# Kernel tuning notes

Hardware: AMD Instinct MI355X
Metric: run time of the kernel (lower is better)

The kernel has to match this reference:

```python
import jax, jax.numpy as jnp
import numpy as np

N, E, IN_F, OUT_F, HEADS = 50000, 800000, 256, 64, 8


def setup_inputs() -> dict:
    key = jax.random.key(0)
    k1, k2, k3, k4, k5 = jax.random.split(key, 5)
    stdv = 1.0 / np.sqrt(OUT_F)
    return {
        "h": jax.random.normal(k1, (N, IN_F), dtype=jnp.float32),
        "weight": jax.random.uniform(k2, (IN_F, OUT_F), minval=-stdv, maxval=stdv, dtype=jnp.float32),
        "attention_w": jax.random.normal(k3, (1, HEADS), dtype=jnp.float32),
        "src": jax.random.randint(k4, (E,), 0, N, dtype=jnp.int32),
        "dst": jax.random.randint(k5, (E,), 0, N, dtype=jnp.int32),
    }


def reference(h, weight, attention_w, src, dst):
    n_nodes = h.shape[0]
    hp = h @ weight                              # [N, F] projected features
    hs = hp[src]                                 # [E, F] gather source feats
    hd = hp[dst]                                 # [E, F] gather dest feats
    dot = jnp.sum(hs * hd, axis=-1, keepdims=True)   # [E, 1] edge dot attention
    # original: (msg[:, F, 1] @ attention_w[1, H]).sum(H) == msg * attention_w.sum()
    msg = dot * hs * jnp.sum(attention_w)        # [E, F]
    accum = jax.ops.segment_sum(msg, dst, num_segments=n_nodes)  # [N, F]
    # DGL update_all: zero in-degree nodes keep their projected feature
    deg = jax.ops.segment_sum(jnp.ones((src.shape[0], 1), hp.dtype), dst, num_segments=n_nodes)
    return jnp.where(deg > 0, accum, hp)
```

## Files before the change

### kernel.cpp

```cpp
#include <hip/hip_runtime.h>

#define IN_F 256
#define OUT_F 64
#define NBKT_MAX 1024
#define PART_BLOCKS 128
#define HIST_BLOCKS 256
#define CAP 3072

typedef __attribute__((ext_vector_type(8))) short short8;
typedef __attribute__((ext_vector_type(4))) float f32x4;
typedef unsigned int uint32;

#define AS_I(f) __builtin_bit_cast(int, f)
#define AS_F(i) __builtin_bit_cast(float, i)
#define DPP_ADD(v, ctrl, rmask) \
    v += AS_F(__builtin_amdgcn_update_dpp(0, AS_I(v), ctrl, rmask, 0xf, true))

__device__ __forceinline__ float half_sum_sel(float p, bool hi) {
    DPP_ADD(p, 0x111, 0xf);
    DPP_ADD(p, 0x112, 0xf);
    DPP_ADD(p, 0x114, 0xf);
    DPP_ADD(p, 0x118, 0xf);
    DPP_ADD(p, 0x142, 0xa);
    float dlo = AS_F(__builtin_amdgcn_readlane(AS_I(p), 31));
    float dhi = AS_F(__builtin_amdgcn_readlane(AS_I(p), 63));
    return hi ? dhi : dlo;
}

__device__ __forceinline__ unsigned short f2bf(float f) {
    uint32 u = __builtin_bit_cast(uint32, f);
    u += 0x7fffu + ((u >> 16) & 1u);
    return (unsigned short)(u >> 16);
}
__device__ __forceinline__ float bf2f(unsigned short s) {
    return __builtin_bit_cast(float, (uint32)s << 16);
}

__global__ __launch_bounds__(256) void gemm_hist_kernel(const float* __restrict__ h,
                                                        const float* __restrict__ w,
                                                        unsigned short* __restrict__ hpb,
                                                        int N,
                                                        const int* __restrict__ dst,
                                                        int* __restrict__ bkt_cnt,
                                                        int E, int NB, int ngemm) {
    __shared__ char smem[32768];
    int b = blockIdx.x, t = threadIdx.x;

    if (b >= ngemm) {
        int* lcnt = (int*)smem;
        int hb = b - ngemm;
        for (int i = t; i < NB; i += 256) lcnt[i] = 0;
        __syncthreads();
        for (int e = hb * 256 + t; e < E; e += HIST_BLOCKS * 256)
            atomicAdd(&lcnt[dst[e] >> 6], 1);
        __syncthreads();
        for (int i = t; i < NB; i += 256)
            if (lcnt[i]) atomicAdd(&bkt_cnt[i], lcnt[i]);
        return;
    }

    short8* wfrag = (short8*)smem;
    for (int slot = t; slot < 2048; slot += 256) {
        int kb = slot >> 6, n = slot & 63;
        short8 v;
#pragma unroll
        for (int jj = 0; jj < 8; ++jj)
            v[jj] = (short)f2bf(w[(size_t)(kb * 8 + jj) * OUT_F + n]);
        wfrag[slot] = v;
    }
    __syncthreads();

    int wave = t >> 6, lane = t & 63;
    int n16  = lane & 15, quad = lane >> 4;
    int base = b * 64 + wave * 16;
    int arow_i = base + n16; if (arow_i >= N) arow_i = N - 1;
    const float* arow = h + (size_t)arow_i * IN_F;

    f32x4 acc[4];
#pragma unroll
    for (int ct = 0; ct < 4; ++ct) acc[ct] = (f32x4){0.f, 0.f, 0.f, 0.f};

#pragma unroll
    for (int ks = 0; ks < 8; ++ks) {
        int k0 = ks * 32;
        float4 a0 = *(const float4*)(arow + k0 + quad * 8);
        float4 a1 = *(const float4*)(arow + k0 + quad * 8 + 4);
        short8 af;
        af[0] = (short)f2bf(a0.x); af[1] = (short)f2bf(a0.y);
        af[2] = (short)f2bf(a0.z); af[3] = (short)f2bf(a0.w);
        af[4] = (short)f2bf(a1.x); af[5] = (short)f2bf(a1.y);
        af[6] = (short)f2bf(a1.z); af[7] = (short)f2bf(a1.w);
        int kb = ks * 4 + quad;
#pragma unroll
        for (int ct = 0; ct < 4; ++ct) {
            short8 bf = wfrag[kb * 64 + ct * 16 + n16];
            acc[ct] = __builtin_amdgcn_mfma_f32_16x16x32_bf16(af, bf, acc[ct], 0, 0, 0);
        }
    }

#pragma unroll
    for (int ct = 0; ct < 4; ++ct) {
#pragma unroll
        for (int r = 0; r < 4; ++r) {
            int ro = base + quad * 4 + r;
            if (ro < N) hpb[(size_t)ro * OUT_F + ct * 16 + n16] = f2bf(acc[ct][r]);
        }
    }
}

__global__ __launch_bounds__(512) void partition_kernel(const int* __restrict__ src,
                                                        const int* __restrict__ dst,
                                                        const int* __restrict__ bkt_cnt,
                                                        int* __restrict__ bkt_cursor,
                                                        int* __restrict__ bkt_base,
                                                        uint32* __restrict__ pairs,
                                                        int E, int NB) {
    __shared__ int sbase[NBKT_MAX + 1];
    __shared__ int lcnt[NBKT_MAX];
    __shared__ int gbase[NBKT_MAX];
    __shared__ int wsum2[8];

    int t = threadIdx.x, lane = t & 63, wid = t >> 6;

    int loc0, loc1;
    int x0 = (t * 2     < NB) ? bkt_cnt[t * 2]     : 0;
    int x1 = (t * 2 + 1 < NB) ? bkt_cnt[t * 2 + 1] : 0;
    loc0 = 0; loc1 = x0;
    int s = x0 + x1;
    int xs = s;
#pragma unroll
    for (int off = 1; off < 64; off <<= 1) {
        int y = __shfl_up(xs, off, 64);
        if (lane >= off) xs += y;
    }
    if (lane == 63) wsum2[wid] = xs;
    __syncthreads();
    int base_w = 0;
    for (int k = 0; k < wid; ++k) base_w += wsum2[k];
    int toff = base_w + xs - s;
    if (t * 2     < NB) sbase[t * 2]     = toff + loc0;
    if (t * 2 + 1 < NB) sbase[t * 2 + 1] = toff + loc1;
    if (t == 0) sbase[NB] = E;
    __syncthreads();

    if (blockIdx.x == 0) {
        for (int i = t; i <= NB; i += 512) bkt_base[i] = sbase[i];
    }

    int chunk = (E + PART_BLOCKS - 1) / PART_BLOCKS;
    int s0 = blockIdx.x * chunk;
    int s1 = min(E, s0 + chunk);

    for (int i = t; i < NB; i += 512) lcnt[i] = 0;
    __syncthreads();
    for (int e = s0 + t; e < s1; e += 512)
        atomicAdd(&lcnt[dst[e] >> 6], 1);
    __syncthreads();
    for (int i = t; i < NB; i += 512) {
        int c = lcnt[i];
        if (c) gbase[i] = sbase[i] + atomicAdd(&bkt_cursor[i], c);
        lcnt[i] = 0;
    }
    __syncthreads();
    for (int e = s0 + t; e < s1; e += 512) {
        int d  = dst[e];
        int bk = d >> 6;
        int idx = atomicAdd(&lcnt[bk], 1);
        pairs[gbase[bk] + idx] = (uint32)src[e] | ((uint32)(d & 63) << 26);
    }
}

#define GATH(S) (*(const uint32*)(hpb + (size_t)(S) * OUT_F + half * 2))
#define PROC(Q) { float a0 = bf2f((unsigned short)((Q) & 0xffff));            \
                  float a1 = bf2f((unsigned short)((Q) >> 16));               \
                  float dd = half_sum_sel(fmaf(a1, hd1, a0 * hd0), hi);       \
                  acc0 = fmaf(dd, a0, acc0); acc1 = fmaf(dd, a1, acc1); }

__global__ __launch_bounds__(512) void accum_sort_kernel(const unsigned short* __restrict__ hpb,
                                                         const uint32* __restrict__ pairs,
                                                         const int* __restrict__ bkt_base,
                                                         const float* __restrict__ attw,
                                                         float* __restrict__ out, int N) {
    __shared__ int slds[CAP];
    __shared__ int bin[64], excl[65], cur[64];

    int b = blockIdx.x, t = threadIdx.x;
    int wid = t >> 6, lane = t & 63;
    int half = lane & 31;
    bool hi  = lane >= 32;
    int node0 = b * 64;

    int beg = bkt_base[b], end = bkt_base[b + 1];
    int nE  = end - beg;

    float c = 0.f;
#pragma unroll
    for (int i = 0; i < 8; ++i) c += attw[i];

    if (nE <= CAP) {
        if (t < 64) bin[t] = 0;
        __syncthreads();
        for (int i = beg + t; i < end; i += 512)
            atomicAdd(&bin[pairs[i] >> 26], 1);
        __syncthreads();
        if (t < 64) {
            int v = bin[t], x = v;
#pragma unroll
            for (int off = 1; off < 64; off <<= 1) {
                int y = __shfl_up(x, off, 64);
                if (t >= off) x += y;
            }
            excl[t] = x - v;
            cur[t]  = x - v;
            if (t == 63) excl[64] = x;
        }
        __syncthreads();
        for (int i = beg + t; i < end; i += 512) {
            uint32 p = pairs[i];
            int dl   = (int)(p >> 26);
            int pos  = atomicAdd(&cur[dl], 1);
            slds[pos] = (int)(p & 0x3FFFFFFu);
        }
        __syncthreads();

#pragma unroll 1
        for (int k = 0; k < 8; ++k) {
            int n    = wid + 8 * k;
            int node = node0 + n;
            if (node >= N) continue;

            int jb = excl[n], je = excl[n + 1];

            uint32 hd2 = *(const uint32*)(hpb + (size_t)node * OUT_F + half * 2);
            float hd0 = bf2f((unsigned short)(hd2 & 0xffff));
            float hd1 = bf2f((unsigned short)(hd2 >> 16));

            float acc0 = 0.f, acc1 = 0.f;
            int j = jb;
            int sel = hi ? 1 : 0;

            for (; j + 16 <= je; j += 16) {
                int i0 = slds[j + 0  + sel], i1 = slds[j + 2  + sel];
                int i2 = slds[j + 4  + sel], i3 = slds[j + 6  + sel];
                int i4 = slds[j + 8  + sel], i5 = slds[j + 10 + sel];
                int i6 = slds[j + 12 + sel], i7 = slds[j + 14 + sel];
                uint32 q0 = GATH(i0), q1 = GATH(i1), q2 = GATH(i2), q3 = GATH(i3);
                uint32 q4 = GATH(i4), q5 = GATH(i5), q6 = GATH(i6), q7 = GATH(i7);
                PROC(q0) PROC(q1) PROC(q2) PROC(q3)
                PROC(q4) PROC(q5) PROC(q6) PROC(q7)
            }
            for (; j + 8 <= je; j += 8) {
                int i0 = slds[j + 0 + sel], i1 = slds[j + 2 + sel];
                int i2 = slds[j + 4 + sel], i3 = slds[j + 6 + sel];
                uint32 q0 = GATH(i0), q1 = GATH(i1), q2 = GATH(i2), q3 = GATH(i3);
                PROC(q0) PROC(q1) PROC(q2) PROC(q3)
            }
            for (; j + 2 <= je; j += 2) {
                int i0 = slds[j + sel];
                uint32 q0 = GATH(i0);
                PROC(q0)
            }
            if (j < je) {
                int i0 = slds[j];
                uint32 q0 = GATH(i0);
                float a0 = bf2f((unsigned short)(q0 & 0xffff));
                float a1 = bf2f((unsigned short)(q0 >> 16));
                float dd = half_sum_sel(fmaf(a1, hd1, a0 * hd0), false);
                if (!hi) {
                    acc0 = fmaf(dd, a0, acc0);
                    acc1 = fmaf(dd, a1, acc1);
                }
            }

            acc0 += __shfl_xor(acc0, 32, 64);
            acc1 += __shfl_xor(acc1, 32, 64);

            if (!hi) {
                float r0, r1;
                if (je > jb) { r0 = acc0 * c; r1 = acc1 * c; }
                else         { r0 = hd0;      r1 = hd1;      }
                *(float2*)(out + (size_t)node * OUT_F + half * 2) = make_float2(r0, r1);
            }
        }
    } else {
#pragma unroll 1
        for (int k = 0; k < 8; ++k) {
            int n    = wid + 8 * k;
            int node = node0 + n;
            if (node >= N) continue;

            uint32 hd2 = *(const uint32*)(hpb + (size_t)node * OUT_F + half * 2);
            float hd0 = bf2f((unsigned short)(hd2 & 0xffff));
            float hd1 = bf2f((unsigned short)(hd2 >> 16));

            float acc0 = 0.f, acc1 = 0.f;
            int deg = 0;
            for (int i = beg; i < end; ++i) {
                uint32 p = pairs[i];
                if ((int)(p >> 26) == n) {
                    ++deg;
                    uint32 q0 = GATH((int)(p & 0x3FFFFFFu));
                    float a0 = bf2f((unsigned short)(q0 & 0xffff));
                    float a1 = bf2f((unsigned short)(q0 >> 16));
                    float dd = half_sum_sel(fmaf(a1, hd1, a0 * hd0), false);
                    if (!hi) {
                        acc0 = fmaf(dd, a0, acc0);
                        acc1 = fmaf(dd, a1, acc1);
                    }
                }
            }
            acc0 += __shfl_xor(acc0, 32, 64);
            acc1 += __shfl_xor(acc1, 32, 64);
            if (!hi) {
                float r0, r1;
                if (deg > 0) { r0 = acc0 * c; r1 = acc1 * c; }
                else         { r0 = hd0;      r1 = hd1;      }
                *(float2*)(out + (size_t)node * OUT_F + half * 2) = make_float2(r0, r1);
            }
        }
    }
}

extern "C" void kernel_launch(void* const* d_in, const int* in_sizes, int n_in,
                              void* d_out, int out_size, void* d_ws, size_t ws_size,
                              hipStream_t stream) {
    const float* h    = (const float*)d_in[0];
    const float* w    = (const float*)d_in[1];
    const float* attw = (const float*)d_in[2];
    const int*   src  = (const int*)d_in[3];
    const int*   dst  = (const int*)d_in[4];

    int N = in_sizes[0] / IN_F;
    int E = in_sizes[3];
    int NB = (N + 63) >> 6;
    int ngemm = (N + 63) / 64;

    float* out = (float*)d_out;

    char* p = (char*)d_ws;
    unsigned short* hpb = (unsigned short*)p;  p += (size_t)N * OUT_F * sizeof(unsigned short);
    int* bkt_cnt    = (int*)p;                 p += (NBKT_MAX + 1) * sizeof(int);
    int* bkt_cursor = (int*)p;                 p += (NBKT_MAX + 1) * sizeof(int);
    int* bkt_base   = (int*)p;                 p += (NBKT_MAX + 1) * sizeof(int);
    uint32* pairs   = (uint32*)p;

    hipMemsetAsync(bkt_cnt, 0, 2 * (NBKT_MAX + 1) * sizeof(int), stream);

    gemm_hist_kernel<<<ngemm + HIST_BLOCKS, 256, 0, stream>>>(h, w, hpb, N,
                                                              dst, bkt_cnt, E, NB, ngemm);

    partition_kernel<<<PART_BLOCKS, 512, 0, stream>>>(src, dst, bkt_cnt, bkt_cursor,
                                                      bkt_base, pairs, E, NB);

    accum_sort_kernel<<<NB, 512, 0, stream>>>(hpb, pairs, bkt_base, attw, out, N);
}
```

Baseline: 154.8 us.

## Fuse partitioning into GEMM kernel with per-block local bucket tables

Replaces the global histogram, memset and separate partition kernel with a block-local partition inside the GEMM launch. Each of the 128 partition blocks sorts its own edge chunk by bucket and writes a per-block offset table. The accumulation kernel then gathers its bucket's 128 segments into LDS using a prefix sum and binary search. This removes a memset and one kernel launch and lets partitioning overlap the GEMM, at the cost of extra table reads and indirection in the accumulate stage.

```diff
diff --git a/kernel.cpp b/kernel.cpp
--- a/kernel.cpp
+++ b/kernel.cpp
@@ -4,7 +4,6 @@
 #define OUT_F 64
 #define NBKT_MAX 1024
 #define PART_BLOCKS 128
-#define HIST_BLOCKS 256
 #define CAP 3072
 
 typedef __attribute__((ext_vector_type(8))) short short8;
@@ -36,29 +35,68 @@
     return __builtin_bit_cast(float, (uint32)s << 16);
 }
 
-__global__ __launch_bounds__(256) void gemm_hist_kernel(const float* __restrict__ h,
+__global__ __launch_bounds__(256) void gemm_part_kernel(const float* __restrict__ h,
                                                         const float* __restrict__ w,
                                                         unsigned short* __restrict__ hpb,
                                                         int N,
+                                                        const int* __restrict__ src,
                                                         const int* __restrict__ dst,
-                                                        int* __restrict__ bkt_cnt,
-                                                        int E, int NB, int ngemm) {
+                                                        int* __restrict__ tbl,
+                                                        uint32* __restrict__ pairs,
+                                                        int E, int NB) {
     __shared__ char smem[32768];
+    __shared__ int wsum[4];
     int b = blockIdx.x, t = threadIdx.x;
 
-    if (b >= ngemm) {
+    if (b < PART_BLOCKS) {
         int* lcnt = (int*)smem;
-        int hb = b - ngemm;
+        int lane = t & 63, wid = t >> 6;
+        int chunk = (E + PART_BLOCKS - 1) / PART_BLOCKS;
+        int s0 = b * chunk, s1 = min(E, s0 + chunk);
+
         for (int i = t; i < NB; i += 256) lcnt[i] = 0;
         __syncthreads();
-        for (int e = hb * 256 + t; e < E; e += HIST_BLOCKS * 256)
+        for (int e = s0 + t; e < s1; e += 256)
             atomicAdd(&lcnt[dst[e] >> 6], 1);
         __syncthreads();
-        for (int i = t; i < NB; i += 256)
-            if (lcnt[i]) atomicAdd(&bkt_cnt[i], lcnt[i]);
+
+        int i0 = t * 4;
+        int x0 = (i0     < NB) ? lcnt[i0]     : 0;
+        int x1 = (i0 + 1 < NB) ? lcnt[i0 + 1] : 0;
+        int x2 = (i0 + 2 < NB) ? lcnt[i0 + 2] : 0;
+        int x3 = (i0 + 3 < NB) ? lcnt[i0 + 3] : 0;
+        int l1 = x0, l2 = x0 + x1, l3 = x0 + x1 + x2;
+        int s  = l3 + x3;
+        int xs = s;
+#pragma unroll
+        for (int off = 1; off < 64; off <<= 1) {
+            int y = __shfl_up(xs, off, 64);
+            if (lane >= off) xs += y;
+        }
+        if (lane == 63) wsum[wid] = xs;
+        __syncthreads();
+        int basew = 0;
+        for (int k = 0; k < wid; ++k) basew += wsum[k];
+        int toff = basew + xs - s;
+
+        int* trow = tbl + (size_t)b * (NB + 1);
+        if (i0     < NB) { trow[i0]     = s0 + toff;      lcnt[i0]     = toff;      }
+        if (i0 + 1 < NB) { trow[i0 + 1] = s0 + toff + l1; lcnt[i0 + 1] = toff + l1; }
+        if (i0 + 2 < NB) { trow[i0 + 2] = s0 + toff + l2; lcnt[i0 + 2] = toff + l2; }
+        if (i0 + 3 < NB) { trow[i0 + 3] = s0 + toff + l3; lcnt[i0 + 3] = toff + l3; }
+        if (t == 0) trow[NB] = s1;
+        __syncthreads();
+
+        for (int e = s0 + t; e < s1; e += 256) {
+            int d  = dst[e];
+            int bk = d >> 6;
+            int idx = atomicAdd(&lcnt[bk], 1);
+            pairs[s0 + idx] = (uint32)src[e] | ((uint32)(d & 63) << 26);
+        }
         return;
     }
 
+    int gb = b - PART_BLOCKS;
     short8* wfrag = (short8*)smem;
     for (int slot = t; slot < 2048; slot += 256) {
         int kb = slot >> 6, n = slot & 63;
@@ -72,7 +110,7 @@
 
     int wave = t >> 6, lane = t & 63;
     int n16  = lane & 15, quad = lane >> 4;
-    int base = b * 64 + wave * 16;
+    int base = gb * 64 + wave * 16;
     int arow_i = base + n16; if (arow_i >= N) arow_i = N - 1;
     const float* arow = h + (size_t)arow_i * IN_F;
 
@@ -108,80 +146,20 @@
     }
 }
 
-__global__ __launch_bounds__(512) void partition_kernel(const int* __restrict__ src,
-                                                        const int* __restrict__ dst,
-                                                        const int* __restrict__ bkt_cnt,
-                                                        int* __restrict__ bkt_cursor,
-                                                        int* __restrict__ bkt_base,
-                                                        uint32* __restrict__ pairs,
-                                                        int E, int NB) {
-    __shared__ int sbase[NBKT_MAX + 1];
-    __shared__ int lcnt[NBKT_MAX];
-    __shared__ int gbase[NBKT_MAX];
-    __shared__ int wsum2[8];
-
-    int t = threadIdx.x, lane = t & 63, wid = t >> 6;
-
-    int loc0, loc1;
-    int x0 = (t * 2     < NB) ? bkt_cnt[t * 2]     : 0;
-    int x1 = (t * 2 + 1 < NB) ? bkt_cnt[t * 2 + 1] : 0;
-    loc0 = 0; loc1 = x0;
-    int s = x0 + x1;
-    int xs = s;
-#pragma unroll
-    for (int off = 1; off < 64; off <<= 1) {
-        int y = __shfl_up(xs, off, 64);
-        if (lane >= off) xs += y;
-    }
-    if (lane == 63) wsum2[wid] = xs;
-    __syncthreads();
-    int base_w = 0;
-    for (int k = 0; k < wid; ++k) base_w += wsum2[k];
-    int toff = base_w + xs - s;
-    if (t * 2     < NB) sbase[t * 2]     = toff + loc0;
-    if (t * 2 + 1 < NB) sbase[t * 2 + 1] = toff + loc1;
-    if (t == 0) sbase[NB] = E;
-    __syncthreads();
-
-    if (blockIdx.x == 0) {
-        for (int i = t; i <= NB; i += 512) bkt_base[i] = sbase[i];
-    }
-
-    int chunk = (E + PART_BLOCKS - 1) / PART_BLOCKS;
-    int s0 = blockIdx.x * chunk;
-    int s1 = min(E, s0 + chunk);
-
-    for (int i = t; i < NB; i += 512) lcnt[i] = 0;
-    __syncthreads();
-    for (int e = s0 + t; e < s1; e += 512)
-        atomicAdd(&lcnt[dst[e] >> 6], 1);
-    __syncthreads();
-    for (int i = t; i < NB; i += 512) {
-        int c = lcnt[i];
-        if (c) gbase[i] = sbase[i] + atomicAdd(&bkt_cursor[i], c);
-        lcnt[i] = 0;
-    }
-    __syncthreads();
-    for (int e = s0 + t; e < s1; e += 512) {
-        int d  = dst[e];
-        int bk = d >> 6;
-        int idx = atomicAdd(&lcnt[bk], 1);
-        pairs[gbase[bk] + idx] = (uint32)src[e] | ((uint32)(d & 63) << 26);
-    }
-}
-
 #define GATH(S) (*(const uint32*)(hpb + (size_t)(S) * OUT_F + half * 2))
 #define PROC(Q) { float a0 = bf2f((unsigned short)((Q) & 0xffff));            \
                   float a1 = bf2f((unsigned short)((Q) >> 16));               \
                   float dd = half_sum_sel(fmaf(a1, hd1, a0 * hd0), hi);       \
                   acc0 = fmaf(dd, a0, acc0); acc1 = fmaf(dd, a1, acc1); }
 
-__global__ __launch_bounds__(512) void accum_sort_kernel(const unsigned short* __restrict__ hpb,
-                                                         const uint32* __restrict__ pairs,
-                                                         const int* __restrict__ bkt_base,
-                                                         const float* __restrict__ attw,
-                                                         float* __restrict__ out, int N) {
+__global__ __launch_bounds__(512) void accum_kernel(const unsigned short* __restrict__ hpb,
+                                                    const uint32* __restrict__ pairs,
+                                                    const int* __restrict__ tbl,
+                                                    const float* __restrict__ attw,
+                                                    float* __restrict__ out, int N, int NB) {
+    __shared__ uint32 sraw[CAP];
     __shared__ int slds[CAP];
+    __shared__ int segb[PART_BLOCKS], slen[PART_BLOCKS], psum[PART_BLOCKS + 1];
     __shared__ int bin[64], excl[65], cur[64];
 
     int b = blockIdx.x, t = threadIdx.x;
@@ -190,18 +168,47 @@
     bool hi  = lane >= 32;
     int node0 = b * 64;
 
-    int beg = bkt_base[b], end = bkt_base[b + 1];
-    int nE  = end - beg;
+    if (t < PART_BLOCKS) {
+        const int* trow = tbl + (size_t)t * (NB + 1);
+        int b0 = trow[b];
+        segb[t] = b0;
+        slen[t] = trow[b + 1] - b0;
+    }
+    __syncthreads();
+    if (wid == 0) {
+        int l0 = slen[lane * 2], l1 = slen[lane * 2 + 1];
+        int s = l0 + l1, xs = s;
+#pragma unroll
+        for (int off = 1; off < 64; off <<= 1) {
+            int y = __shfl_up(xs, off, 64);
+            if (lane >= off) xs += y;
+        }
+        int ex = xs - s;
+        psum[lane * 2]     = ex;
+        psum[lane * 2 + 1] = ex + l0;
+        if (lane == 63) psum[PART_BLOCKS] = xs;
+    }
+    __syncthreads();
+    int nE = psum[PART_BLOCKS];
 
     float c = 0.f;
 #pragma unroll
     for (int i = 0; i < 8; ++i) c += attw[i];
 
     if (nE <= CAP) {
+        for (int i = t; i < nE; i += 512) {
+            int lo = 0, hh = PART_BLOCKS - 1;
+#pragma unroll
+            for (int it = 0; it < 7; ++it) {
+                int mid = (lo + hh + 1) >> 1;
+                if (psum[mid] <= i) lo = mid; else hh = mid - 1;
+            }
+            sraw[i] = pairs[segb[lo] + (i - psum[lo])];
+        }
         if (t < 64) bin[t] = 0;
         __syncthreads();
-        for (int i = beg + t; i < end; i += 512)
-            atomicAdd(&bin[pairs[i] >> 26], 1);
+        for (int i = t; i < nE; i += 512)
+            atomicAdd(&bin[sraw[i] >> 26], 1);
         __syncthreads();
         if (t < 64) {
             int v = bin[t], x = v;
@@ -215,10 +222,9 @@
             if (t == 63) excl[64] = x;
         }
         __syncthreads();
-        for (int i = beg + t; i < end; i += 512) {
-            uint32 p = pairs[i];
-            int dl   = (int)(p >> 26);
-            int pos  = atomicAdd(&cur[dl], 1);
+        for (int i = t; i < nE; i += 512) {
+            uint32 p = sraw[i];
+            int pos = atomicAdd(&cur[(int)(p >> 26)], 1);
             slds[pos] = (int)(p & 0x3FFFFFFu);
         }
         __syncthreads();
@@ -295,17 +301,20 @@
 
             float acc0 = 0.f, acc1 = 0.f;
             int deg = 0;
-            for (int i = beg; i < end; ++i) {
-                uint32 p = pairs[i];
-                if ((int)(p >> 26) == n) {
-                    ++deg;
-                    uint32 q0 = GATH((int)(p & 0x3FFFFFFu));
-                    float a0 = bf2f((unsigned short)(q0 & 0xffff));
-                    float a1 = bf2f((unsigned short)(q0 >> 16));
-                    float dd = half_sum_sel(fmaf(a1, hd1, a0 * hd0), false);
-                    if (!hi) {
-                        acc0 = fmaf(dd, a0, acc0);
-                        acc1 = fmaf(dd, a1, acc1);
+            for (int p = 0; p < PART_BLOCKS; ++p) {
+                int bb = segb[p], ee = bb + slen[p];
+                for (int i = bb; i < ee; ++i) {
+                    uint32 pr = pairs[i];
+                    if ((int)(pr >> 26) == n) {
+                        ++deg;
+                        uint32 q0 = GATH((int)(pr & 0x3FFFFFFu));
+                        float a0 = bf2f((unsigned short)(q0 & 0xffff));
+                        float a1 = bf2f((unsigned short)(q0 >> 16));
+                        float dd = half_sum_sel(fmaf(a1, hd1, a0 * hd0), false);
+                        if (!hi) {
+                            acc0 = fmaf(dd, a0, acc0);
+                            acc1 = fmaf(dd, a1, acc1);
+                        }
                     }
                 }
             }
@@ -339,18 +348,11 @@
 
     char* p = (char*)d_ws;
     unsigned short* hpb = (unsigned short*)p;  p += (size_t)N * OUT_F * sizeof(unsigned short);
-    int* bkt_cnt    = (int*)p;                 p += (NBKT_MAX + 1) * sizeof(int);
-    int* bkt_cursor = (int*)p;                 p += (NBKT_MAX + 1) * sizeof(int);
-    int* bkt_base   = (int*)p;                 p += (NBKT_MAX + 1) * sizeof(int);
-    uint32* pairs   = (uint32*)p;
-
-    hipMemsetAsync(bkt_cnt, 0, 2 * (NBKT_MAX + 1) * sizeof(int), stream);
-
-    gemm_hist_kernel<<<ngemm + HIST_BLOCKS, 256, 0, stream>>>(h, w, hpb, N,
-                                                              dst, bkt_cnt, E, NB, ngemm);
-
-    partition_kernel<<<PART_BLOCKS, 512, 0, stream>>>(src, dst, bkt_cnt, bkt_cursor,
-                                                      bkt_base, pairs, E, NB);
-
-    accum_sort_kernel<<<NB, 512, 0, stream>>>(hpb, pairs, bkt_base, attw, out, N);
-}
+    int* tbl      = (int*)p;                   p += (size_t)PART_BLOCKS * (NBKT_MAX + 1) * sizeof(int);
+    uint32* pairs = (uint32*)p;
+
+    gemm_part_kernel<<<PART_BLOCKS + ngemm, 256, 0, stream>>>(h, w, hpb, N,
+                                                              src, dst, tbl, pairs, E, NB);
+
+    accum_kernel<<<NB, 512, 0, stream>>>(hpb, pairs, tbl, attw, out, N, NB);
+}
```

Measured after the change: 147.9 us. 1.05x faster.
